# Optimization experiments

Measured on AMD Instinct MI355X. Metric: run time of the kernel, lower is better.

Reference implementation:

```python
import jax, jax.numpy as jnp
import numpy as np

H = 100
N = 262144

def setup_inputs() -> dict:
    key = jax.random.key(0)
    ks = jax.random.split(key, 9)
    s = 1.0 / np.sqrt(H)
    return {
        "m": jax.random.normal(ks[0], (1, H), jnp.float32),
        "output_hidden": jax.random.normal(ks[1], (1, 1, H), jnp.float32),
        "fact_embeddings": jax.random.normal(ks[2], (N, H), jnp.float32),
        "W1": jax.random.normal(ks[3], (H, 2 * H), jnp.float32) * s,
        "b1": jax.random.normal(ks[4], (H,), jnp.float32) * s,
        "W2": jax.random.normal(ks[5], (1, H), jnp.float32) * s,
        "b2": jax.random.normal(ks[6], (1,), jnp.float32) * s,
        "W3": jax.random.normal(ks[7], (H, 3 * H), jnp.float32) * s,
        "b3": jax.random.normal(ks[8], (H,), jnp.float32) * s,
    }

def reference(m, output_hidden, fact_embeddings, W1, b1, W2, b2, W3, b3):
    output_context = output_hidden[0]                      # [1, H]
    # z = [|f - oh| ; |f - m|]  -> [N, 2H] (broadcast over N)
    z = jnp.concatenate(
        [jnp.abs(fact_embeddings - output_context),
         jnp.abs(fact_embeddings - m)], axis=1)
    # MLP attention scores, softmax over N facts
    g = jnp.tanh(z @ W1.T + b1) @ W2.T + b2                # [N, 1]
    g = jax.nn.softmax(g.ravel())                          # [N]
    # Weighted-sum pooling of facts
    c = (g[:, None] * fact_embeddings).sum(axis=0, keepdims=True)  # [1, H]
    # Gated memory update
    m_new = jax.nn.relu(jnp.concatenate([m, c, output_context], axis=1) @ W3.T + b3)
    return m_new
```

## Files before the change

kernel.cpp:

```cpp
#include <hip/hip_runtime.h>
#include <hip/hip_bf16.h>
#include <math.h>

#define HDIM 100
#define NFACT 262144
#define FPB   128
#define NBLK_T 2048
#define TPB   4
#define GRID  (NBLK_T / TPB)
#define NTHREADS 512

#define KHALF 112
#define NJT 7
#define NKC 7
#define NBFRAG (NJT * NKC * 64)

#define NCOPY 116
#define NSTRIPE 4

using short8 = __attribute__((ext_vector_type(8))) short;
using f32x4  = __attribute__((ext_vector_type(4))) float;

#define WS_B    0
#define WS_ACC  12544

__device__ __forceinline__ unsigned short f2bf(float x) {
    unsigned u = __builtin_bit_cast(unsigned, x);
    u += 0x7FFFu + ((u >> 16) & 1u);
    return (unsigned short)(u >> 16);
}

__device__ __forceinline__ float tanh_fast(float x) {
    float e = __expf(2.0f * x);
    return 1.0f - 2.0f / (1.0f + e);
}

__global__ __launch_bounds__(256) void k_prep_b(const float* __restrict__ W1,
                                                float* __restrict__ ws) {
    int tg = blockIdx.x * 256 + threadIdx.x;
    if (tg < NSTRIPE * NCOPY) ws[WS_ACC + tg] = 0.f;
    if (tg >= NBFRAG) return;
    int lane = tg & 63;
    int kc = (tg >> 6) % NKC;
    int jt = tg / (NKC * 64);
    int g = lane >> 4, r = lane & 15;
    int j = jt * 16 + r;
    unsigned short v[8];
    #pragma unroll
    for (int e = 0; e < 8; e++) {
        int kglob = kc * 32 + g * 8 + e;
        int half = (kglob >= KHALF) ? 1 : 0;
        int koff = kglob - half * KHALF;
        float x = 0.f;
        if (j < HDIM && koff < HDIM) x = W1[j * 200 + half * HDIM + koff];
        v[e] = f2bf(x);
    }
    uint4 d;
    d.x = (unsigned)v[0] | ((unsigned)v[1] << 16);
    d.y = (unsigned)v[2] | ((unsigned)v[3] << 16);
    d.z = (unsigned)v[4] | ((unsigned)v[5] << 16);
    d.w = (unsigned)v[6] | ((unsigned)v[7] << 16);
    ((uint4*)(ws + WS_B))[tg] = d;
}

__device__ __forceinline__ float4 ld4c(const float* p, bool ok) {
    float4 z = make_float4(0.f, 0.f, 0.f, 0.f);
    return ok ? *(const float4*)p : z;
}

__device__ __forceinline__ uint4 pack_diff_u(float4 a0, float4 a1,
                                             float4 b0, float4 b1) {
    union { __hip_bfloat16 h[8]; uint4 u; } u;
    u.h[0] = __float2bfloat16(a0.x - b0.x); u.h[1] = __float2bfloat16(a0.y - b0.y);
    u.h[2] = __float2bfloat16(a0.z - b0.z); u.h[3] = __float2bfloat16(a0.w - b0.w);
    u.h[4] = __float2bfloat16(a1.x - b1.x); u.h[5] = __float2bfloat16(a1.y - b1.y);
    u.h[6] = __float2bfloat16(a1.z - b1.z); u.h[7] = __float2bfloat16(a1.w - b1.w);
    return u.u;
}

__device__ __forceinline__ uint4 and_mask(uint4 u) {
    u.x &= 0x7FFF7FFFu; u.y &= 0x7FFF7FFFu;
    u.z &= 0x7FFF7FFFu; u.w &= 0x7FFF7FFFu;
    return u;
}

__device__ __forceinline__ float4 shfl32_f4(float4 v) {
    float4 r;
    r.x = __shfl_xor(v.x, 32); r.y = __shfl_xor(v.y, 32);
    r.z = __shfl_xor(v.z, 32); r.w = __shfl_xor(v.w, 32);
    return r;
}

template<int CTRL>
__device__ __forceinline__ float dpp_radd(float x) {
    int y = __builtin_amdgcn_update_dpp(0, __builtin_bit_cast(int, x),
                                        CTRL, 0xF, 0xF, true);
    return x + __builtin_bit_cast(float, y);
}
__device__ __forceinline__ float row_reduce16(float x) {
    x = dpp_radd<0x121>(x);
    x = dpp_radd<0x122>(x);
    x = dpp_radd<0x124>(x);
    x = dpp_radd<0x128>(x);
    return x;
}

__global__ __launch_bounds__(NTHREADS, 2) void k_logits(
        const float* __restrict__ fe,
        const float* __restrict__ oc,
        const float* __restrict__ mvec,
        const float* __restrict__ b1,
        const float* __restrict__ W2,
        float* __restrict__ ws) {
    __shared__ __align__(16) uint4 Bs[NBFRAG];
    __shared__ float poolS[KHALF];
    __shared__ float cpad[2 * KHALF];
    __shared__ float bw[2 * KHALF];
    __shared__ float sS;

    int t = threadIdx.x;
    int w = t >> 6, lane = t & 63, g = lane >> 4, r = lane & 15;
    bool ghi = (lane & 32) != 0;

    if (t == 0) sS = 0.f;
    if (t < KHALF) poolS[t] = 0.f;

    if (t < 2 * KHALF) {
        int half = t / KHALF, k = t % KHALF;
        cpad[t] = (k < HDIM) ? (half ? mvec[k] : oc[k]) : 0.f;
        bw[t]   = (k < HDIM) ? (half ? W2[k]   : b1[k]) : 0.f;
    }

    {
        const uint4* Bg = (const uint4*)(ws + WS_B);
        #pragma unroll
        for (int i = 0; i < 7; i++) {
            int base = i * 512 + w * 64;
            if (base < NBFRAG) {
                __builtin_amdgcn_global_load_lds(
                    (const __attribute__((address_space(1))) unsigned int*)(Bg + base + lane),
                    (__attribute__((address_space(3))) unsigned int*)(Bs + base),
                    16, 0, 0);
            }
        }
    }

    int row_off = w * 16 + r;

    auto issue_load = [&](int tile, float4* f0, float4* f1) {
        const float* fp = fe + ((long)tile * FPB + row_off) * HDIM;
        if (tile != NBLK_T - 1) {
            #pragma unroll
            for (int kc = 0; kc < 4; kc++) {
                int pk = kc * 32 + g * 8;
                int col = (pk >= KHALF) ? (pk - KHALF) : pk;
                f0[kc] = *(const float4*)(fp + col);
                f1[kc] = *(const float4*)(fp + col + 4);
            }
        } else {
            #pragma unroll
            for (int kc = 0; kc < 4; kc++) {
                int pk = kc * 32 + g * 8;
                int col = (pk >= KHALF) ? (pk - KHALF) : pk;
                f0[kc] = ld4c(fp + col, col < HDIM);
                f1[kc] = ld4c(fp + col + 4, col + 4 < HDIM);
            }
        }
    };

    float sacc = 0.f;

    auto process = [&](float4* f0c, float4* f1c) {
        uint4 zsig[4];
        #pragma unroll
        for (int kc = 0; kc < 4; kc++) {
            int pk = kc * 32 + g * 8;
            float4 s0 = *(const float4*)(cpad + pk);
            float4 s1 = *(const float4*)(cpad + pk + 4);
            zsig[kc] = pack_diff_u(f0c[kc], f1c[kc], s0, s1);
        }
        uint4 zabsHi[3];
        #pragma unroll
        for (int c = 0; c < 3; c++) {
            int pk = (4 + c) * 32 + g * 8;
            float4 sa0 = ghi ? f0c[c] : f0c[c + 1];
            float4 sa1 = ghi ? f1c[c] : f1c[c + 1];
            float4 ra0 = shfl32_f4(sa0);
            float4 ra1 = shfl32_f4(sa1);
            float4 s0 = *(const float4*)(cpad + pk);
            float4 s1 = *(const float4*)(cpad + pk + 4);
            zabsHi[c] = and_mask(pack_diff_u(ra0, ra1, s0, s1));
        }

        float gacc = 0.f;
        #pragma unroll
        for (int jt = 0; jt < NJT; jt++) {
            int jb = jt * 16 + g * 4;
            float4 b1q = *(const float4*)(bw + jb);
            float4 w2q = *(const float4*)(bw + KHALF + jb);
            f32x4 acc = {b1q.x, b1q.y, b1q.z, b1q.w};
            #pragma unroll
            for (int kc = 0; kc < NKC; kc++) {
                short8 av = __builtin_bit_cast(short8, Bs[(jt * NKC + kc) * 64 + lane]);
                uint4 bu = (kc < 4) ? and_mask(zsig[kc]) : zabsHi[kc - 4];
                acc = __builtin_amdgcn_mfma_f32_16x16x32_bf16(
                    av, __builtin_bit_cast(short8, bu), acc, 0, 0, 0);
            }
            gacc = fmaf(tanh_fast(acc[0]), w2q.x, gacc);
            gacc = fmaf(tanh_fast(acc[1]), w2q.y, gacc);
            gacc = fmaf(tanh_fast(acc[2]), w2q.z, gacc);
            gacc = fmaf(tanh_fast(acc[3]), w2q.w, gacc);
        }
        gacc += __shfl_xor(gacc, 16);
        gacc += __shfl_xor(gacc, 32);
        float w_r = __expf(gacc);
        sacc += w_r;

        float p[4][8];
        #pragma unroll
        for (int c = 0; c < 4; c++) {
            union { uint4 u; unsigned short us[8]; } uz; uz.u = zsig[c];
            #pragma unroll
            for (int e = 0; e < 8; e++) {
                float zf = __builtin_bit_cast(float, ((unsigned)uz.us[e]) << 16);
                p[c][e] = w_r * zf;
            }
        }
        #pragma unroll
        for (int c = 0; c < 4; c++)
            #pragma unroll
            for (int e = 0; e < 8; e++) p[c][e] = row_reduce16(p[c][e]);
        if (r == 0) {
            #pragma unroll
            for (int c = 0; c < 4; c++) {
                int pk = c * 32 + g * 8;
                if (pk < KHALF) {
                    #pragma unroll
                    for (int e = 0; e < 8; e++)
                        atomicAdd(&poolS[pk + e], p[c][e]);
                }
            }
        }
    };

    int tile0 = blockIdx.x * TPB;
    float4 fA0[4], fA1[4], fB0[4], fB1[4];

    issue_load(tile0 + 0, fA0, fA1);
    __syncthreads();

    issue_load(tile0 + 1, fB0, fB1);
    process(fA0, fA1);
    __builtin_amdgcn_sched_barrier(0);

    issue_load(tile0 + 2, fA0, fA1);
    process(fB0, fB1);
    __builtin_amdgcn_sched_barrier(0);

    issue_load(tile0 + 3, fB0, fB1);
    process(fA0, fA1);
    __builtin_amdgcn_sched_barrier(0);

    process(fB0, fB1);

    float s16 = row_reduce16(sacc);
    if (lane == 0) atomicAdd(&sS, s16);
    __syncthreads();

    int cp = (blockIdx.x & (NSTRIPE - 1)) * NCOPY;
    if (t < KHALF && t < HDIM) atomicAdd(&ws[WS_ACC + cp + t], poolS[t]);
    if (t == 0) atomicAdd(&ws[WS_ACC + cp + KHALF], sS);
}

__global__ __launch_bounds__(128) void k_final(
        const float* __restrict__ mvec,
        const float* __restrict__ oc,
        const float* __restrict__ W3,
        const float* __restrict__ b3,
        const float* __restrict__ ws,
        float* __restrict__ out) {
    __shared__ float vv[300];
    int t = threadIdx.x;
    float S = 0.f;
    #pragma unroll
    for (int i = 0; i < NSTRIPE; i++) S += ws[WS_ACC + i * NCOPY + KHALF];
    if (t < HDIM) {
        float corr = 0.f;
        #pragma unroll
        for (int i = 0; i < NSTRIPE; i++) corr += ws[WS_ACC + i * NCOPY + t];
        vv[t] = mvec[t];
        vv[HDIM + t] = oc[t] + corr / S;
        vv[2 * HDIM + t] = oc[t];
    }
    __syncthreads();
    if (t < HDIM) {
        float a = b3[t];
        const float* wr = W3 + t * 3 * HDIM;
        #pragma unroll 4
        for (int k = 0; k < 3 * HDIM; k++) a = fmaf(wr[k], vv[k], a);
        out[t] = fmaxf(a, 0.f);
    }
}

extern "C" void kernel_launch(void* const* d_in, const int* in_sizes, int n_in,
                              void* d_out, int out_size, void* d_ws, size_t ws_size,
                              hipStream_t stream) {
    const float* mvec = (const float*)d_in[0];
    const float* oh   = (const float*)d_in[1];
    const float* fe   = (const float*)d_in[2];
    const float* W1   = (const float*)d_in[3];
    const float* b1   = (const float*)d_in[4];
    const float* W2   = (const float*)d_in[5];
    const float* W3   = (const float*)d_in[7];
    const float* b3   = (const float*)d_in[8];
    float* ws  = (float*)d_ws;
    float* out = (float*)d_out;

    k_prep_b<<<13, 256, 0, stream>>>(W1, ws);
    k_logits<<<GRID, NTHREADS, 0, stream>>>(fe, oh, mvec, b1, W2, ws);
    k_final<<<1, 128, 0, stream>>>(mvec, oh, W3, b3, ws, out);
}
```

Baseline: 75.62 us.

## Process two fact tiles per pass with interleaved MFMA chains and merged pooling

Restructures the per-block loop so two tiles are built and then scored together. Their MFMA accumulations, tanh reductions and exp run interleaved to expose instruction-level parallelism, and their weighted contributions are combined before the cross-lane reduction and shared atomics, halving those. The cost is weaker load/compute overlap: the next pair's loads are issued just before use rather than while the previous tile is processed. Register pressure also rises.

```diff
diff --git a/kernel.cpp b/kernel.cpp
--- a/kernel.cpp
+++ b/kernel.cpp
@@ -168,10 +168,7 @@
         }
     };
 
-    float sacc = 0.f;
-
-    auto process = [&](float4* f0c, float4* f1c) {
-        uint4 zsig[4];
+    auto build = [&](float4* f0c, float4* f1c, uint4* zsig, uint4* zhi) {
         #pragma unroll
         for (int kc = 0; kc < 4; kc++) {
             int pk = kc * 32 + g * 8;
@@ -179,7 +176,6 @@
             float4 s1 = *(const float4*)(cpad + pk + 4);
             zsig[kc] = pack_diff_u(f0c[kc], f1c[kc], s0, s1);
         }
-        uint4 zabsHi[3];
         #pragma unroll
         for (int c = 0; c < 3; c++) {
             int pk = (4 + c) * 32 + g * 8;
@@ -189,79 +185,86 @@
             float4 ra1 = shfl32_f4(sa1);
             float4 s0 = *(const float4*)(cpad + pk);
             float4 s1 = *(const float4*)(cpad + pk + 4);
-            zabsHi[c] = and_mask(pack_diff_u(ra0, ra1, s0, s1));
-        }
-
-        float gacc = 0.f;
+            zhi[c] = and_mask(pack_diff_u(ra0, ra1, s0, s1));
+        }
+    };
+
+    float sacc = 0.f;
+
+    auto process_dual = [&](uint4* zsA, uint4* zhA, uint4* zsB, uint4* zhB) {
+        float gA = 0.f, gB = 0.f;
         #pragma unroll
         for (int jt = 0; jt < NJT; jt++) {
             int jb = jt * 16 + g * 4;
             float4 b1q = *(const float4*)(bw + jb);
             float4 w2q = *(const float4*)(bw + KHALF + jb);
-            f32x4 acc = {b1q.x, b1q.y, b1q.z, b1q.w};
+            f32x4 accA = {b1q.x, b1q.y, b1q.z, b1q.w};
+            f32x4 accB = accA;
             #pragma unroll
             for (int kc = 0; kc < NKC; kc++) {
                 short8 av = __builtin_bit_cast(short8, Bs[(jt * NKC + kc) * 64 + lane]);
-                uint4 bu = (kc < 4) ? and_mask(zsig[kc]) : zabsHi[kc - 4];
-                acc = __builtin_amdgcn_mfma_f32_16x16x32_bf16(
-                    av, __builtin_bit_cast(short8, bu), acc, 0, 0, 0);
-            }
-            gacc = fmaf(tanh_fast(acc[0]), w2q.x, gacc);
-            gacc = fmaf(tanh_fast(acc[1]), w2q.y, gacc);
-            gacc = fmaf(tanh_fast(acc[2]), w2q.z, gacc);
-            gacc = fmaf(tanh_fast(acc[3]), w2q.w, gacc);
-        }
-        gacc += __shfl_xor(gacc, 16);
-        gacc += __shfl_xor(gacc, 32);
-        float w_r = __expf(gacc);
-        sacc += w_r;
-
-        float p[4][8];
+                uint4 buA = (kc < 4) ? and_mask(zsA[kc]) : zhA[kc - 4];
+                uint4 buB = (kc < 4) ? and_mask(zsB[kc]) : zhB[kc - 4];
+                accA = __builtin_amdgcn_mfma_f32_16x16x32_bf16(
+                    av, __builtin_bit_cast(short8, buA), accA, 0, 0, 0);
+                accB = __builtin_amdgcn_mfma_f32_16x16x32_bf16(
+                    av, __builtin_bit_cast(short8, buB), accB, 0, 0, 0);
+            }
+            gA = fmaf(tanh_fast(accA[0]), w2q.x, gA);
+            gB = fmaf(tanh_fast(accB[0]), w2q.x, gB);
+            gA = fmaf(tanh_fast(accA[1]), w2q.y, gA);
+            gB = fmaf(tanh_fast(accB[1]), w2q.y, gB);
+            gA = fmaf(tanh_fast(accA[2]), w2q.z, gA);
+            gB = fmaf(tanh_fast(accB[2]), w2q.z, gB);
+            gA = fmaf(tanh_fast(accA[3]), w2q.w, gA);
+            gB = fmaf(tanh_fast(accB[3]), w2q.w, gB);
+        }
+        gA += __shfl_xor(gA, 16); gB += __shfl_xor(gB, 16);
+        gA += __shfl_xor(gA, 32); gB += __shfl_xor(gB, 32);
+        float wA = __expf(gA);
+        float wB = __expf(gB);
+        sacc += wA + wB;
+
         #pragma unroll
         for (int c = 0; c < 4; c++) {
-            union { uint4 u; unsigned short us[8]; } uz; uz.u = zsig[c];
+            union { uint4 u; unsigned short us[8]; } uA, uB;
+            uA.u = zsA[c]; uB.u = zsB[c];
+            float p[8];
             #pragma unroll
             for (int e = 0; e < 8; e++) {
-                float zf = __builtin_bit_cast(float, ((unsigned)uz.us[e]) << 16);
-                p[c][e] = w_r * zf;
-            }
-        }
-        #pragma unroll
-        for (int c = 0; c < 4; c++)
-            #pragma unroll
-            for (int e = 0; e < 8; e++) p[c][e] = row_reduce16(p[c][e]);
-        if (r == 0) {
-            #pragma unroll
-            for (int c = 0; c < 4; c++) {
-                int pk = c * 32 + g * 8;
-                if (pk < KHALF) {
-                    #pragma unroll
-                    for (int e = 0; e < 8; e++)
-                        atomicAdd(&poolS[pk + e], p[c][e]);
-                }
+                float zA = __builtin_bit_cast(float, ((unsigned)uA.us[e]) << 16);
+                float zB = __builtin_bit_cast(float, ((unsigned)uB.us[e]) << 16);
+                p[e] = fmaf(wA, zA, wB * zB);
+            }
+            #pragma unroll
+            for (int e = 0; e < 8; e++) p[e] = row_reduce16(p[e]);
+            int pk = c * 32 + g * 8;
+            if (r == 0 && pk < KHALF) {
+                #pragma unroll
+                for (int e = 0; e < 8; e++)
+                    atomicAdd(&poolS[pk + e], p[e]);
             }
         }
     };
 
     int tile0 = blockIdx.x * TPB;
     float4 fA0[4], fA1[4], fB0[4], fB1[4];
+    uint4 zsA[4], zhA[3], zsB[4], zhB[3];
 
     issue_load(tile0 + 0, fA0, fA1);
+    issue_load(tile0 + 1, fB0, fB1);
     __syncthreads();
-
-    issue_load(tile0 + 1, fB0, fB1);
-    process(fA0, fA1);
+    build(fA0, fA1, zsA, zhA);
+    build(fB0, fB1, zsB, zhB);
+    process_dual(zsA, zhA, zsB, zhB);
     __builtin_amdgcn_sched_barrier(0);
 
     issue_load(tile0 + 2, fA0, fA1);
-    process(fB0, fB1);
+    issue_load(tile0 + 3, fB0, fB1);
+    build(fA0, fA1, zsA, zhA);
+    build(fB0, fB1, zsB, zhB);
+    process_dual(zsA, zhA, zsB, zhB);
     __builtin_amdgcn_sched_barrier(0);
-
-    issue_load(tile0 + 3, fB0, fB1);
-    process(fA0, fA1);
-    __builtin_amdgcn_sched_barrier(0);
-
-    process(fB0, fB1);
 
     float s16 = row_reduce16(sacc);
     if (lane == 0) atomicAdd(&sS, s16);
```

After: 78.23 us. +3.5%, slower.
